# Optimization experiments

Hardware: AMD Instinct MI355X
Metric: run time of the kernel (lower is better)

The kernel has to match this reference:

```python
import jax, jax.numpy as jnp
import numpy as np

NUM_HEADS = 8

def setup_inputs() -> dict:
    key = jax.random.key(0)
    ks = jax.random.split(key, 7)
    B, N, K, C = 4, 16384, 16, 64
    pcd = jax.random.normal(ks[0], (B, C, N), dtype=jnp.float32)
    neighbors = jax.random.normal(ks[1], (B, C, N, K), dtype=jnp.float32)
    xyz = jax.random.normal(ks[2], (B, 3, N), dtype=jnp.float32)
    idx_all = jax.random.randint(ks[3], (B, N, K), 0, N)
    Wq = jax.random.normal(ks[4], (C, C + 3), dtype=jnp.float32) * 0.1
    Wk = jax.random.normal(ks[5], (C, C + 3), dtype=jnp.float32) * 0.1
    Wv = jax.random.normal(ks[6], (C, C + 3), dtype=jnp.float32) * 0.1
    return {"pcd": pcd, "neighbors": neighbors, "xyz": xyz,
            "Wq": Wq, "Wk": Wk, "Wv": Wv, "idx_all": idx_all}


def reference(pcd, neighbors, xyz, Wq, Wk, Wv, idx_all):
    B, C, N = pcd.shape
    K = neighbors.shape[-1]
    H = NUM_HEADS
    D = C // H
    # --- query: concat xyz, 1x1 conv, split heads ---
    pcd_cat = jnp.concatenate([pcd, xyz], axis=1)                 # (B, C+3, N)
    q = jnp.einsum('oc,bcn->bon', Wq, pcd_cat)                    # (B, C, N)
    q = q.reshape(B, H, D, N).transpose(0, 1, 3, 2)               # (B, H, N, D)
    # --- index_points: gather xyz at KNN indices (irregular gather) ---
    xyz_t = xyz.transpose(0, 2, 1)                                # (B, N, 3)
    rel_xyz = jax.vmap(lambda pts, ix: pts[ix])(xyz_t, idx_all)   # (B, N, K, 3)
    nb = jnp.concatenate([neighbors, rel_xyz.transpose(0, 3, 1, 2)], axis=1)  # (B, C+3, N, K)
    # --- key/value: 1x1 conv + split heads ---
    k = jnp.einsum('oc,bcnk->bonk', Wk, nb).reshape(B, H, D, N, K).transpose(0, 1, 3, 4, 2)  # (B,H,N,K,D)
    v = jnp.einsum('oc,bcnk->bonk', Wv, nb).reshape(B, H, D, N, K).transpose(0, 1, 3, 4, 2)  # (B,H,N,K,D)
    # --- local scalar-dot attention over the K neighbors of each point ---
    energy = jnp.einsum('bhnd,bhnkd->bhnk', q, k) / jnp.sqrt(jnp.float32(D))  # (B,H,N,K)
    attn = jax.nn.softmax(energy, axis=-1)
    x = jnp.einsum('bhnk,bhnkd->bhnd', attn, v)                   # (B, H, N, D)
    # (B,H,N,D) -> (B,N,H*D) -> (B, C, N), matching torch reshape/permute order
    out = x.transpose(0, 2, 1, 3).reshape(B, N, H * D).transpose(0, 2, 1)
    return out
```

## Files before the change

kernel.cpp:

```cpp
#include <hip/hip_runtime.h>
#include <math.h>

#define B_ 4
#define C_ 64
#define N_ 16384
#define K_ 16
#define H_ 8
#define CP 67
#define CPAD 68
#define NP 16
#define QSTRIDE 65
#define ESTRIDE 552

__device__ __align__(16) float wpad[3 * C_ * CPAD];

__global__ void setup_weights(const float* __restrict__ Wq,
                              const float* __restrict__ Wk,
                              const float* __restrict__ Wv) {
  int i = blockIdx.x * blockDim.x + threadIdx.x;
  if (i >= C_ * CPAD) return;
  int o = i / CPAD, j = i - o * CPAD;
  float q = 0.f, kk = 0.f, v = 0.f;
  if (j < CP) {
    q = Wq[o * CP + j] * 0.35355339059327373f;
    kk = Wk[o * CP + j];
    v = Wv[o * CP + j];
  }
  wpad[i] = q;
  wpad[C_ * CPAD + i] = kk;
  wpad[2 * C_ * CPAD + i] = v;
}

#define SWZ(v, imm) __int_as_float(__builtin_amdgcn_ds_swizzle(__float_as_int(v), (imm)))
#define XOR1 0x041F
#define XOR2 0x081F
#define XOR4 0x101F
#define XOR8 0x201F

__launch_bounds__(256, 3)
__global__ void pt_attn(const float* __restrict__ pcd,
                        const float* __restrict__ neighbors,
                        const float* __restrict__ xyz,
                        const int* __restrict__ idx_all,
                        float* __restrict__ out) {
  __shared__ __align__(16) float x_lds[NP * CPAD];
  __shared__ float q_lds[NP * QSTRIDE];
  __shared__ __align__(16) float e_lds[NP * ESTRIDE];

  const int tid = threadIdx.x;
  const int p = tid >> 4;
  const int k = tid & 15;
  const int blk = blockIdx.x;
  const int b = blk >> 10;
  const int n0 = (blk & 1023) << 4;
  const int n = n0 + p;

  float nb[CPAD];
  {
    const float* gp = neighbors + (size_t)b * (C_ * N_ * K_) + n0 * K_ + tid;
#pragma unroll
    for (int c = 0; c < C_; ++c)
      nb[c] = gp[(size_t)c * (N_ * K_)];
  }
  {
    const int idx = idx_all[(b * N_ + n) * K_ + k];
    const float* gx = xyz + (size_t)b * (3 * N_) + idx;
    nb[64] = gx[0];
    nb[65] = gx[N_];
    nb[66] = gx[2 * N_];
    nb[67] = 0.f;
  }

  {
    const int pp = tid & 15;
    const int c0 = tid >> 4;
#pragma unroll
    for (int it = 0; it < 4; ++it) {
      int c = c0 + it * 16;
      x_lds[pp * CPAD + c] = pcd[((size_t)b * C_ + c) * N_ + n0 + pp];
    }
    if (tid < 48)
      x_lds[pp * CPAD + 64 + c0] = xyz[((size_t)b * 3 + c0) * N_ + n0 + pp];
    if (tid < 16)
      x_lds[pp * CPAD + 67] = 0.f;
  }
  __syncthreads();

  {
    const float4* xr = (const float4*)(x_lds + p * CPAD);
    const float4* wq = (const float4*)(wpad) + 4 * k * 17;
    float a0 = 0.f, a1 = 0.f, a2 = 0.f, a3 = 0.f;
#pragma unroll
    for (int j4 = 0; j4 < 17; ++j4) {
      float4 xv = xr[j4];
      float4 w0 = wq[j4];
      float4 w1 = wq[17 + j4];
      float4 w2 = wq[34 + j4];
      float4 w3 = wq[51 + j4];
      a0 += w0.x * xv.x + w0.y * xv.y + w0.z * xv.z + w0.w * xv.w;
      a1 += w1.x * xv.x + w1.y * xv.y + w1.z * xv.z + w1.w * xv.w;
      a2 += w2.x * xv.x + w2.y * xv.y + w2.z * xv.z + w2.w * xv.w;
      a3 += w3.x * xv.x + w3.y * xv.y + w3.z * xv.z + w3.w * xv.w;
    }
    q_lds[p * QSTRIDE + 4 * k + 0] = a0;
    q_lds[p * QSTRIDE + 4 * k + 1] = a1;
    q_lds[p * QSTRIDE + 4 * k + 2] = a2;
    q_lds[p * QSTRIDE + 4 * k + 3] = a3;
  }
  __syncthreads();

  {
    const int h = k & 7;
    const int jh = k >> 3;
    float qa[8];
#pragma unroll
    for (int d = 0; d < 8; ++d)
      qa[d] = q_lds[p * QSTRIDE + h * 8 + d];
    const float4* wk = (const float4*)(wpad + C_ * CPAD) + h * 8 * 17;
    float4* er = (float4*)(e_lds + p * ESTRIDE + h * CPAD);
#pragma unroll
    for (int u = 0; u < 9; ++u) {
      int j4 = jh * 8 + u;
      float4 a = make_float4(0.f, 0.f, 0.f, 0.f);
#pragma unroll
      for (int d = 0; d < 8; ++d) {
        float4 w = wk[d * 17 + j4];
        a.x += qa[d] * w.x;
        a.y += qa[d] * w.y;
        a.z += qa[d] * w.z;
        a.w += qa[d] * w.w;
      }
      er[j4] = a;
    }
  }
  __syncthreads();

  float en[8];
#pragma unroll
  for (int h = 0; h < 8; ++h) en[h] = 0.f;
  {
    const float4* ep = (const float4*)(e_lds + p * ESTRIDE);
#pragma unroll
    for (int j4 = 0; j4 < 17; ++j4) {
#pragma unroll
      for (int h = 0; h < 8; ++h) {
        float4 e4 = ep[h * 17 + j4];
        en[h] += e4.x * nb[4 * j4 + 0] + e4.y * nb[4 * j4 + 1] +
                 e4.z * nb[4 * j4 + 2] + e4.w * nb[4 * j4 + 3];
      }
    }
  }
  float at[8];
#pragma unroll
  for (int h = 0; h < 8; ++h) {
    float m = en[h];
    m = fmaxf(m, SWZ(m, XOR1));
    m = fmaxf(m, SWZ(m, XOR2));
    m = fmaxf(m, SWZ(m, XOR4));
    m = fmaxf(m, SWZ(m, XOR8));
    float e = __expf(en[h] - m);
    float s = e;
    s += SWZ(s, XOR1);
    s += SWZ(s, XOR2);
    s += SWZ(s, XOR4);
    s += SWZ(s, XOR8);
    at[h] = e * __builtin_amdgcn_rcpf(s);
  }

  float ap[8];
  {
    const bool g2 = (k & 8) != 0;
    const bool g1 = (k & 4) != 0;
    const bool g0 = (k & 2) != 0;
    float t0[8], t1[8];
#pragma unroll
    for (int i = 0; i < 8; ++i) t0[i] = g2 ? at[i ^ 4] : at[i];
#pragma unroll
    for (int i = 0; i < 8; ++i) t1[i] = g1 ? t0[i ^ 2] : t0[i];
#pragma unroll
    for (int i = 0; i < 8; ++i) ap[i] = g0 ? t1[i ^ 1] : t1[i];
  }

  float xo0 = 0.f, xo1 = 0.f, xo2 = 0.f, xo3 = 0.f;
  const float4* wv = (const float4*)(wpad + 2 * C_ * CPAD) + 4 * k * 17;
#pragma unroll
  for (int j4 = 0; j4 < 17; ++j4) {
    float agg0, agg1, agg2, agg3;
#pragma unroll
    for (int u = 0; u < 4; ++u) {
      float nbj = nb[4 * j4 + u];
      float s0 = ap[0] * nbj, s1 = ap[1] * nbj, s2 = ap[2] * nbj, s3 = ap[3] * nbj;
      float s4 = ap[4] * nbj, s5 = ap[5] * nbj, s6 = ap[6] * nbj, s7 = ap[7] * nbj;
      s0 += SWZ(s4, XOR8);
      s1 += SWZ(s5, XOR8);
      s2 += SWZ(s6, XOR8);
      s3 += SWZ(s7, XOR8);
      s0 += SWZ(s2, XOR4);
      s1 += SWZ(s3, XOR4);
      s0 += SWZ(s1, XOR2);
      s0 += SWZ(s0, XOR1);
      if (u == 0) agg0 = s0;
      else if (u == 1) agg1 = s0;
      else if (u == 2) agg2 = s0;
      else agg3 = s0;
    }
    float4 w0 = wv[j4];
    float4 w1 = wv[17 + j4];
    float4 w2 = wv[34 + j4];
    float4 w3 = wv[51 + j4];
    xo0 += w0.x * agg0 + w0.y * agg1 + w0.z * agg2 + w0.w * agg3;
    xo1 += w1.x * agg0 + w1.y * agg1 + w1.z * agg2 + w1.w * agg3;
    xo2 += w2.x * agg0 + w2.y * agg1 + w2.z * agg2 + w2.w * agg3;
    xo3 += w3.x * agg0 + w3.y * agg1 + w3.z * agg2 + w3.w * agg3;
  }

  float* op = out + ((size_t)b * C_ + 4 * k) * N_ + n0 + p;
  op[0] = xo0;
  op[(size_t)N_] = xo1;
  op[2 * (size_t)N_] = xo2;
  op[3 * (size_t)N_] = xo3;
}

extern "C" void kernel_launch(void* const* d_in, const int* in_sizes, int n_in,
                              void* d_out, int out_size, void* d_ws, size_t ws_size,
                              hipStream_t stream) {
  const float* pcd = (const float*)d_in[0];
  const float* neighbors = (const float*)d_in[1];
  const float* xyz = (const float*)d_in[2];
  const float* Wq = (const float*)d_in[3];
  const float* Wk = (const float*)d_in[4];
  const float* Wv = (const float*)d_in[5];
  const int* idx = (const int*)d_in[6];
  float* out = (float*)d_out;

  setup_weights<<<(C_ * CPAD + 255) / 256, 256, 0, stream>>>(Wq, Wk, Wv);
  pt_attn<<<B_ * (N_ / NP), 256, 0, stream>>>(pcd, neighbors, xyz, idx, out);
}
```

Before: 630.4 us.

## Use DPP quad permutes, cut LDS footprint, and raise occupancy to four blocks

Merges the three shared arrays into one aliased buffer, reading q into registers before the energy stage overwrites it, so more blocks fit per CU, and raises launch bounds to 4 blocks. The energy dot product now reads only two heads' rows per lane and broadcasts the rest with DPP quad_perm, instead of reading all eight heads from LDS. Most ds_swizzle butterfly steps become cheaper DPP moves, and the head-to-lane mapping and output channel assignment are remapped to match. The tighter register budget at higher occupancy risks spilling the 68-float neighbor array.

```diff
diff --git a/kernel.cpp b/kernel.cpp
--- a/kernel.cpp
+++ b/kernel.cpp
@@ -5,12 +5,12 @@
 #define C_ 64
 #define N_ 16384
 #define K_ 16
-#define H_ 8
 #define CP 67
 #define CPAD 68
 #define NP 16
+#define ESTRIDE 548
+#define QOFF 1088
 #define QSTRIDE 65
-#define ESTRIDE 552
 
 __device__ __align__(16) float wpad[3 * C_ * CPAD];
 
@@ -32,20 +32,35 @@
 }
 
 #define SWZ(v, imm) __int_as_float(__builtin_amdgcn_ds_swizzle(__float_as_int(v), (imm)))
-#define XOR1 0x041F
-#define XOR2 0x081F
-#define XOR4 0x101F
-#define XOR8 0x201F
-
-__launch_bounds__(256, 3)
+#define XOR4S 0x101F
+#define XOR8S 0x201F
+
+#define DPPF(v, ctrl) \
+  __int_as_float(__builtin_amdgcn_mov_dpp(__float_as_int(v), (ctrl), 0xF, 0xF, 0))
+#define QP_XOR1 0xB1
+#define QP_XOR2 0x4E
+
+template <int CTRL>
+__device__ __forceinline__ float qbc(float v) {
+  return __int_as_float(__builtin_amdgcn_mov_dpp(__float_as_int(v), CTRL, 0xF, 0xF, 0));
+}
+
+template <int M>
+__device__ __forceinline__ void mac2(float& enE, float& enO, float4 a, float4 b,
+                                     float x0, float x1, float x2, float x3) {
+  enE += qbc<M * 0x55>(a.x) * x0 + qbc<M * 0x55>(a.y) * x1 +
+         qbc<M * 0x55>(a.z) * x2 + qbc<M * 0x55>(a.w) * x3;
+  enO += qbc<M * 0x55>(b.x) * x0 + qbc<M * 0x55>(b.y) * x1 +
+         qbc<M * 0x55>(b.z) * x2 + qbc<M * 0x55>(b.w) * x3;
+}
+
+__launch_bounds__(256, 4)
 __global__ void pt_attn(const float* __restrict__ pcd,
                         const float* __restrict__ neighbors,
                         const float* __restrict__ xyz,
                         const int* __restrict__ idx_all,
                         float* __restrict__ out) {
-  __shared__ __align__(16) float x_lds[NP * CPAD];
-  __shared__ float q_lds[NP * QSTRIDE];
-  __shared__ __align__(16) float e_lds[NP * ESTRIDE];
+  __shared__ __align__(16) float smem[NP * ESTRIDE];
 
   const int tid = threadIdx.x;
   const int p = tid >> 4;
@@ -77,17 +92,17 @@
 #pragma unroll
     for (int it = 0; it < 4; ++it) {
       int c = c0 + it * 16;
-      x_lds[pp * CPAD + c] = pcd[((size_t)b * C_ + c) * N_ + n0 + pp];
+      smem[pp * CPAD + c] = pcd[((size_t)b * C_ + c) * N_ + n0 + pp];
     }
     if (tid < 48)
-      x_lds[pp * CPAD + 64 + c0] = xyz[((size_t)b * 3 + c0) * N_ + n0 + pp];
+      smem[pp * CPAD + 64 + c0] = xyz[((size_t)b * 3 + c0) * N_ + n0 + pp];
     if (tid < 16)
-      x_lds[pp * CPAD + 67] = 0.f;
-  }
-  __syncthreads();
-
-  {
-    const float4* xr = (const float4*)(x_lds + p * CPAD);
+      smem[pp * CPAD + 67] = 0.f;
+  }
+  __syncthreads();
+
+  {
+    const float4* xr = (const float4*)(smem + p * CPAD);
     const float4* wq = (const float4*)(wpad) + 4 * k * 17;
     float a0 = 0.f, a1 = 0.f, a2 = 0.f, a3 = 0.f;
 #pragma unroll
@@ -102,22 +117,24 @@
       a2 += w2.x * xv.x + w2.y * xv.y + w2.z * xv.z + w2.w * xv.w;
       a3 += w3.x * xv.x + w3.y * xv.y + w3.z * xv.z + w3.w * xv.w;
     }
-    q_lds[p * QSTRIDE + 4 * k + 0] = a0;
-    q_lds[p * QSTRIDE + 4 * k + 1] = a1;
-    q_lds[p * QSTRIDE + 4 * k + 2] = a2;
-    q_lds[p * QSTRIDE + 4 * k + 3] = a3;
-  }
-  __syncthreads();
-
-  {
-    const int h = k & 7;
+    smem[QOFF + p * QSTRIDE + 4 * k + 0] = a0;
+    smem[QOFF + p * QSTRIDE + 4 * k + 1] = a1;
+    smem[QOFF + p * QSTRIDE + 4 * k + 2] = a2;
+    smem[QOFF + p * QSTRIDE + 4 * k + 3] = a3;
+  }
+  __syncthreads();
+
+  const int h_ = k & 7;
+  float qa[8];
+#pragma unroll
+  for (int d = 0; d < 8; ++d)
+    qa[d] = smem[QOFF + p * QSTRIDE + h_ * 8 + d];
+  __syncthreads();
+
+  {
     const int jh = k >> 3;
-    float qa[8];
-#pragma unroll
-    for (int d = 0; d < 8; ++d)
-      qa[d] = q_lds[p * QSTRIDE + h * 8 + d];
-    const float4* wk = (const float4*)(wpad + C_ * CPAD) + h * 8 * 17;
-    float4* er = (float4*)(e_lds + p * ESTRIDE + h * CPAD);
+    const float4* wk = (const float4*)(wpad + C_ * CPAD) + h_ * 8 * 17;
+    float4* er = (float4*)(smem + p * ESTRIDE + h_ * CPAD);
 #pragma unroll
     for (int u = 0; u < 9; ++u) {
       int j4 = jh * 8 + u;
@@ -139,50 +156,55 @@
 #pragma unroll
   for (int h = 0; h < 8; ++h) en[h] = 0.f;
   {
-    const float4* ep = (const float4*)(e_lds + p * ESTRIDE);
+    const float* e0 = smem + p * ESTRIDE + (2 * (k & 3)) * CPAD;
 #pragma unroll
     for (int j4 = 0; j4 < 17; ++j4) {
-#pragma unroll
-      for (int h = 0; h < 8; ++h) {
-        float4 e4 = ep[h * 17 + j4];
-        en[h] += e4.x * nb[4 * j4 + 0] + e4.y * nb[4 * j4 + 1] +
-                 e4.z * nb[4 * j4 + 2] + e4.w * nb[4 * j4 + 3];
-      }
-    }
-  }
+      float4 a = *(const float4*)(e0 + 4 * j4);
+      float4 bq = *(const float4*)(e0 + CPAD + 4 * j4);
+      float x0 = nb[4 * j4 + 0], x1 = nb[4 * j4 + 1];
+      float x2 = nb[4 * j4 + 2], x3 = nb[4 * j4 + 3];
+      mac2<0>(en[0], en[1], a, bq, x0, x1, x2, x3);
+      mac2<1>(en[2], en[3], a, bq, x0, x1, x2, x3);
+      mac2<2>(en[4], en[5], a, bq, x0, x1, x2, x3);
+      mac2<3>(en[6], en[7], a, bq, x0, x1, x2, x3);
+    }
+  }
+
   float at[8];
 #pragma unroll
   for (int h = 0; h < 8; ++h) {
     float m = en[h];
-    m = fmaxf(m, SWZ(m, XOR1));
-    m = fmaxf(m, SWZ(m, XOR2));
-    m = fmaxf(m, SWZ(m, XOR4));
-    m = fmaxf(m, SWZ(m, XOR8));
+    m = fmaxf(m, DPPF(m, QP_XOR1));
+    m = fmaxf(m, DPPF(m, QP_XOR2));
+    m = fmaxf(m, SWZ(m, XOR4S));
+    m = fmaxf(m, SWZ(m, XOR8S));
     float e = __expf(en[h] - m);
     float s = e;
-    s += SWZ(s, XOR1);
-    s += SWZ(s, XOR2);
-    s += SWZ(s, XOR4);
-    s += SWZ(s, XOR8);
+    s += DPPF(s, QP_XOR1);
+    s += DPPF(s, QP_XOR2);
+    s += SWZ(s, XOR4S);
+    s += SWZ(s, XOR8S);
     at[h] = e * __builtin_amdgcn_rcpf(s);
   }
 
   float ap[8];
   {
-    const bool g2 = (k & 8) != 0;
-    const bool g1 = (k & 4) != 0;
-    const bool g0 = (k & 2) != 0;
+    const bool c4 = (k & 1) != 0;
+    const bool c2 = (k & 2) != 0;
+    const bool c1 = (k & 4) != 0;
     float t0[8], t1[8];
 #pragma unroll
-    for (int i = 0; i < 8; ++i) t0[i] = g2 ? at[i ^ 4] : at[i];
-#pragma unroll
-    for (int i = 0; i < 8; ++i) t1[i] = g1 ? t0[i ^ 2] : t0[i];
-#pragma unroll
-    for (int i = 0; i < 8; ++i) ap[i] = g0 ? t1[i ^ 1] : t1[i];
-  }
-
+    for (int i = 0; i < 8; ++i) t0[i] = c4 ? at[i ^ 4] : at[i];
+#pragma unroll
+    for (int i = 0; i < 8; ++i) t1[i] = c2 ? t0[i ^ 2] : t0[i];
+#pragma unroll
+    for (int i = 0; i < 8; ++i) ap[i] = c1 ? t1[i ^ 1] : t1[i];
+  }
+
+  const int gk = ((k & 1) << 2) | (k & 2) | ((k & 4) >> 2);
+  const int o_base = (gk << 3) | ((k >> 3) << 2);
   float xo0 = 0.f, xo1 = 0.f, xo2 = 0.f, xo3 = 0.f;
-  const float4* wv = (const float4*)(wpad + 2 * C_ * CPAD) + 4 * k * 17;
+  const float4* wv = (const float4*)(wpad + 2 * C_ * CPAD) + o_base * 17;
 #pragma unroll
   for (int j4 = 0; j4 < 17; ++j4) {
     float agg0, agg1, agg2, agg3;
@@ -191,14 +213,14 @@
       float nbj = nb[4 * j4 + u];
       float s0 = ap[0] * nbj, s1 = ap[1] * nbj, s2 = ap[2] * nbj, s3 = ap[3] * nbj;
       float s4 = ap[4] * nbj, s5 = ap[5] * nbj, s6 = ap[6] * nbj, s7 = ap[7] * nbj;
-      s0 += SWZ(s4, XOR8);
-      s1 += SWZ(s5, XOR8);
-      s2 += SWZ(s6, XOR8);
-      s3 += SWZ(s7, XOR8);
-      s0 += SWZ(s2, XOR4);
-      s1 += SWZ(s3, XOR4);
-      s0 += SWZ(s1, XOR2);
-      s0 += SWZ(s0, XOR1);
+      s0 += DPPF(s4, QP_XOR1);
+      s1 += DPPF(s5, QP_XOR1);
+      s2 += DPPF(s6, QP_XOR1);
+      s3 += DPPF(s7, QP_XOR1);
+      s0 += DPPF(s2, QP_XOR2);
+      s1 += DPPF(s3, QP_XOR2);
+      s0 += SWZ(s1, XOR4S);
+      s0 += SWZ(s0, XOR8S);
       if (u == 0) agg0 = s0;
       else if (u == 1) agg1 = s0;
       else if (u == 2) agg2 = s0;
@@ -214,7 +236,7 @@
     xo3 += w3.x * agg0 + w3.y * agg1 + w3.z * agg2 + w3.w * agg3;
   }
 
-  float* op = out + ((size_t)b * C_ + 4 * k) * N_ + n0 + p;
+  float* op = out + ((size_t)b * C_ + o_base) * N_ + n0 + p;
   op[0] = xo0;
   op[(size_t)N_] = xo1;
   op[2 * (size_t)N_] = xo2;
```

After: 1.288 ms. 2.04x slower.
